# Optimization experiments

Measured on AMD Instinct MI355X. Metric: run time of the kernel, lower is better.

The kernel has to match this reference:

```python
import jax, jax.numpy as jnp
import numpy as np
from jax import lax

B = 8; IMG = 224; P = 16; D = 192; DEPTH = 8
H = IMG // P; W = H; L = H * W
D_IN = 384; D_STATE = 16; D_CONV = 4; DT_R = 12; NCLS = 1000
EPS = 1e-5


def _ln(x, w, b):
    m = x.mean(-1, keepdims=True)
    v = ((x - m) ** 2).mean(-1, keepdims=True)
    return (x - m) * lax.rsqrt(v + EPS) * w + b


def _mixer(seq, p):
    # seq: (B, L, D) -> Mamba selective-scan mixer
    xz = jnp.einsum('bld,ed->ble', seq, p['in_proj_w'])  # (B,L,2*D_IN)
    u, z = jnp.split(xz, 2, axis=-1)
    # causal depthwise conv1d over L
    uc = lax.conv_general_dilated(u.transpose(0, 2, 1), p['conv_w'][:, None, :], (1,),
                                  [(D_CONV - 1, 0)], feature_group_count=D_IN,
                                  dimension_numbers=('NCH', 'OIH', 'NCH'))
    u = jax.nn.silu(uc.transpose(0, 2, 1) + p['conv_b'])
    xdbl = jnp.einsum('bld,ed->ble', u, p['x_proj_w'])  # (B,L,DT_R+2*D_STATE)
    dt = xdbl[..., :DT_R]
    Bm = xdbl[..., DT_R:DT_R + D_STATE]
    Cm = xdbl[..., DT_R + D_STATE:]
    delta = jax.nn.softplus(jnp.einsum('blr,dr->bld', dt, p['dt_w']) + p['dt_b'])
    A = -jnp.exp(p['A_log'])  # (D_IN, D_STATE)

    def step(h, inp):
        d_t, B_t, C_t, u_t = inp  # (b,D_IN),(b,N),(b,N),(b,D_IN)
        h = h * jnp.exp(d_t[..., None] * A) + (d_t * u_t)[..., None] * B_t[:, None, :]
        return h, jnp.einsum('bdn,bn->bd', h, C_t)

    h0 = jnp.zeros((seq.shape[0], D_IN, D_STATE), seq.dtype)
    _, ys = lax.scan(step, h0, (delta.transpose(1, 0, 2), Bm.transpose(1, 0, 2),
                                Cm.transpose(1, 0, 2), u.transpose(1, 0, 2)))
    y = ys.transpose(1, 0, 2) + u * p['D']
    y = y * jax.nn.silu(z)
    return jnp.einsum('bld,cd->blc', y, p['out_proj_w'])


def _stack(seq, params):
    # Block: residual = residual + hidden; hidden = mixer(LN(residual))
    def body(carry, p):
        hidden, residual = carry
        residual = residual + hidden
        hidden = _mixer(_ln(residual, p['ln_w'], p['ln_b']), p)
        return (hidden, residual), None

    (hidden, residual), _ = lax.scan(body, (seq, jnp.zeros_like(seq)), params)
    return hidden + residual


def _forward(x, patch_w, patch_b, pe_ln_w, pe_ln_b, ln_w, ln_b, in_proj_w, conv_w,
             conv_b, x_proj_w, dt_w, dt_b, A_log, Dp, out_proj_w, out_norm_w,
             out_norm_b, head_ln_w, head_ln_b, head_w, head_b):
    b = x.shape[0]
    # patch embed: conv(stride=patch) + LayerNorm over channels
    feat = lax.conv_general_dilated(x, patch_w, (P, P), 'VALID',
                                    dimension_numbers=('NCHW', 'OIHW', 'NCHW'))
    feat = feat + patch_b[None, :, None, None]  # (B, D, H, W)
    feat = _ln(feat.transpose(0, 2, 3, 1), pe_ln_w, pe_ln_b).transpose(0, 3, 1, 2)
    # CrossScan: 4 directional unrollings
    x0 = feat.reshape(b, D, L)
    x1 = feat.transpose(0, 1, 3, 2).reshape(b, D, L)
    xs = jnp.stack([x0, x1, x0[..., ::-1], x1[..., ::-1]], axis=1)  # (B,4,D,L)
    dirs = xs.transpose(1, 0, 3, 2)  # (4,B,L,D)
    params = {'ln_w': ln_w, 'ln_b': ln_b, 'in_proj_w': in_proj_w, 'conv_w': conv_w,
              'conv_b': conv_b, 'x_proj_w': x_proj_w, 'dt_w': dt_w, 'dt_b': dt_b,
              'A_log': A_log, 'D': Dp, 'out_proj_w': out_proj_w}
    outs = jax.vmap(_stack)(dirs, params)  # (4,B,L,D)
    # CrossMerge
    ys = outs.transpose(1, 0, 3, 2)  # (B,4,D,L)
    ym = ys[:, 0:2] + ys[:, 2:4][..., ::-1]
    y = ym[:, 0] + ym[:, 1].reshape(b, D, W, H).transpose(0, 1, 3, 2).reshape(b, D, L)
    y = _ln(y.transpose(0, 2, 1), out_norm_w, out_norm_b)  # (B,L,D)
    y = _ln(y.reshape(b, H, W, D), head_ln_w, head_ln_b)
    return y.mean(axis=(1, 2)) @ head_w.T + head_b  # (B, NCLS)


def setup_inputs() -> dict:
    key = jax.random.key(0)
    ks = jax.random.split(key, 10)
    rn = lambda k, s, sc=0.02: jax.random.normal(k, s, jnp.float32) * sc
    A_init = jnp.broadcast_to(jnp.arange(1, D_STATE + 1, dtype=jnp.float32),
                              (4, DEPTH, D_IN, D_STATE))
    return {
        'x': jax.random.normal(ks[0], (B, 3, IMG, IMG), jnp.float32),
        'patch_w': rn(ks[1], (D, 3, P, P)),
        'patch_b': jnp.zeros((D,), jnp.float32),
        'pe_ln_w': jnp.ones((D,), jnp.float32),
        'pe_ln_b': jnp.zeros((D,), jnp.float32),
        'ln_w': jnp.ones((4, DEPTH, D), jnp.float32),
        'ln_b': jnp.zeros((4, DEPTH, D), jnp.float32),
        'in_proj_w': rn(ks[2], (4, DEPTH, 2 * D_IN, D)),
        'conv_w': rn(ks[3], (4, DEPTH, D_IN, D_CONV), 0.1),
        'conv_b': jnp.zeros((4, DEPTH, D_IN), jnp.float32),
        'x_proj_w': rn(ks[4], (4, DEPTH, DT_R + 2 * D_STATE, D_IN)),
        'dt_w': rn(ks[5], (4, DEPTH, D_IN, DT_R), 0.1),
        'dt_b': jnp.log(jnp.expm1(0.01)) + rn(ks[6], (4, DEPTH, D_IN), 0.02),
        'A_log': jnp.log(A_init),
        'Dp': jnp.ones((4, DEPTH, D_IN), jnp.float32),
        'out_proj_w': rn(ks[7], (4, DEPTH, D, D_IN)),
        'out_norm_w': jnp.ones((D,), jnp.float32),
        'out_norm_b': jnp.zeros((D,), jnp.float32),
        'head_ln_w': jnp.ones((D,), jnp.float32),
        'head_ln_b': jnp.zeros((D,), jnp.float32),
        'head_w': rn(ks[8], (NCLS, D)),
        'head_b': jnp.zeros((NCLS,), jnp.float32),
    }


def reference(x, patch_w, patch_b, pe_ln_w, pe_ln_b, ln_w, ln_b, in_proj_w, conv_w,
              conv_b, x_proj_w, dt_w, dt_b, A_log, Dp, out_proj_w, out_norm_w,
              out_norm_b, head_ln_w, head_ln_b, head_w, head_b):
    return _forward(x, patch_w, patch_b, pe_ln_w, pe_ln_b, ln_w, ln_b, in_proj_w,
                    conv_w, conv_b, x_proj_w, dt_w, dt_b, A_log, Dp, out_proj_w,
                    out_norm_w, out_norm_b, head_ln_w, head_ln_b, head_w, head_b)
```

## Files before the change

kernel.cpp:

```cpp
#include <hip/hip_runtime.h>

#define B_ 8
#define IMGSZ 224
#define PATCH 16
#define D_ 192
#define DEPTH_ 8
#define H_ 14
#define W_ 14
#define L_ 196
#define DIN 384
#define DSTATE 16
#define DCONV 4
#define DTR 12
#define NCLS_ 1000
#define EPS_ 1e-5f
#define ROWS_PER_DIR (B_*L_)
#define M_TOTAL (4*ROWS_PER_DIR)

typedef unsigned short ushort_t;
typedef unsigned int uint_t;
typedef __attribute__((ext_vector_type(8)))  short bf16x8;
typedef __attribute__((ext_vector_type(16))) float f32x16;

__device__ __forceinline__ ushort_t f2bf(float f) {
  uint_t u = __builtin_bit_cast(uint_t, f);
  u += 0x7fffu + ((u >> 16) & 1u);
  return (ushort_t)(u >> 16);
}
__device__ __forceinline__ float bf2f(ushort_t s) {
  uint_t u = ((uint_t)s) << 16;
  return __builtin_bit_cast(float, u);
}

__global__ __launch_bounds__(256) void k_cvt3(
    const float* __restrict__ s0, const float* __restrict__ s1,
    const float* __restrict__ s2, ushort_t* __restrict__ dst)
{
  int i = blockIdx.x*256 + threadIdx.x;
  if (i >= 1806336) return;
  const float* src;
  int off;
  if (i < 36864)        { src = s0; off = i; }
  else if (i < 1216512) { src = s1; off = i - 36864; }
  else                  { src = s2; off = i - 1216512; }
  float4 v = reinterpret_cast<const float4*>(src)[off];
  ushort4 o;
  o.x = f2bf(v.x); o.y = f2bf(v.y); o.z = f2bf(v.z); o.w = f2bf(v.w);
  reinterpret_cast<ushort4*>(dst)[i] = o;
}

__global__ __launch_bounds__(256) void k_cvt_xw(const float* __restrict__ src,
                                                ushort_t* __restrict__ dst)
{
  int idx = blockIdx.x*256 + threadIdx.x;
  if (idx >= 32*64*384) return;
  int g = idx / (64*384);
  int r = (idx / 384) % 64;
  int k = idx % 384;
  float v = (r < 44) ? src[((size_t)g*44 + r)*384 + k] : 0.f;
  dst[idx] = f2bf(v);
}

__global__ __launch_bounds__(256) void k_im2col(const float* __restrict__ x,
                                                ushort_t* __restrict__ Xp)
{
  int idx = blockIdx.x*256 + threadIdx.x;
  if (idx >= ROWS_PER_DIR*768) return;
  int row = idx / 768, k = idx - row*768;
  int b = row / L_, l = row - b*L_;
  int hh = l / W_, ww = l - hh*W_;
  int c = k >> 8, rem = k & 255, pi = rem >> 4, pj = rem & 15;
  float v = x[(((size_t)b*3 + c)*IMGSZ + hh*PATCH + pi)*IMGSZ + ww*PATCH + pj];
  Xp[idx] = f2bf(v);
}

template<int KT, int OBF>
__global__ __launch_bounds__(64) void k_gemm2(
    const ushort_t* __restrict__ X, const ushort_t* __restrict__ W,
    void* __restrict__ C, int N, int nb, int wstride, int rows_per_dir)
{
  int row0 = blockIdx.x*32, col0 = blockIdx.y*64;
  int dir = row0 / rows_per_dir;
  const ushort_t* Wp = W + (size_t)dir*wstride;
  int l = threadIdx.x;
  int r31 = l & 31, khalf = (l >> 5)*8;
  const ushort_t* aptr  = X  + (size_t)(row0 + r31)*KT + khalf;
  const ushort_t* b0ptr = Wp + (size_t)(col0 + r31)*KT + khalf;
  const ushort_t* b1ptr = b0ptr + (size_t)32*KT;
  f32x16 acc00 = {}, acc01 = {}, acc10 = {}, acc11 = {};
  #pragma unroll
  for (int k = 0; k < KT; k += 32) {
    bf16x8 a0 = *reinterpret_cast<const bf16x8*>(aptr + k);
    bf16x8 a1 = *reinterpret_cast<const bf16x8*>(aptr + k + 16);
    bf16x8 b00 = *reinterpret_cast<const bf16x8*>(b0ptr + k);
    bf16x8 b01 = *reinterpret_cast<const bf16x8*>(b0ptr + k + 16);
    bf16x8 b10 = *reinterpret_cast<const bf16x8*>(b1ptr + k);
    bf16x8 b11 = *reinterpret_cast<const bf16x8*>(b1ptr + k + 16);
    acc00 = __builtin_amdgcn_mfma_f32_32x32x16_bf16(a0, b00, acc00, 0, 0, 0);
    acc01 = __builtin_amdgcn_mfma_f32_32x32x16_bf16(a1, b01, acc01, 0, 0, 0);
    acc10 = __builtin_amdgcn_mfma_f32_32x32x16_bf16(a0, b10, acc10, 0, 0, 0);
    acc11 = __builtin_amdgcn_mfma_f32_32x32x16_bf16(a1, b11, acc11, 0, 0, 0);
  }
  int c0 = col0 + r31, c1 = col0 + 32 + r31;
  #pragma unroll
  for (int r = 0; r < 16; ++r) {
    int row = (r & 3) + 8*(r >> 2) + 4*(l >> 5);
    size_t base = (size_t)(row0 + row)*N;
    float v0 = acc00[r] + acc01[r];
    float v1 = acc10[r] + acc11[r];
    if (OBF) {
      ushort_t* crow = (ushort_t*)C + base;
      if (c0 < nb) crow[c0] = f2bf(v0);
      if (c1 < nb) crow[c1] = f2bf(v1);
    } else {
      float* crow = (float*)C + base;
      if (c0 < nb) crow[c0] = v0;
      if (c1 < nb) crow[c1] = v1;
    }
  }
}

__global__ __launch_bounds__(64) void k_peln(
    const float* __restrict__ Cp, const float* __restrict__ pb,
    const float* __restrict__ plw, const float* __restrict__ plb,
    const float* __restrict__ lnw, const float* __restrict__ lnb,
    float* __restrict__ residual, ushort_t* __restrict__ xln)
{
  int blk = blockIdx.x;
  int b = blk / L_, l = blk - b*L_;
  int hh = l / W_, ww = l - hh*W_;
  int lane = threadIdx.x;
  float v[3]; float s = 0.f;
  #pragma unroll
  for (int i = 0; i < 3; ++i) {
    int d = lane + i*64;
    float t = Cp[(size_t)blk*D_ + d] + pb[d];
    v[i] = t; s += t;
  }
  #pragma unroll
  for (int off = 32; off; off >>= 1) s += __shfl_xor(s, off);
  float m = s*(1.f/D_); float q = 0.f;
  #pragma unroll
  for (int i = 0; i < 3; ++i) { float dd = v[i]-m; q += dd*dd; }
  #pragma unroll
  for (int off = 32; off; off >>= 1) q += __shfl_xor(q, off);
  float inv = rsqrtf(q*(1.f/D_)+EPS_);
  float nv[3]; s = 0.f;
  #pragma unroll
  for (int i = 0; i < 3; ++i) {
    int d = lane + i*64;
    nv[i] = (v[i]-m)*inv*plw[d] + plb[d];
    s += nv[i];
  }
  #pragma unroll
  for (int off = 32; off; off >>= 1) s += __shfl_xor(s, off);
  float m2 = s*(1.f/D_); q = 0.f;
  #pragma unroll
  for (int i = 0; i < 3; ++i) { float dd = nv[i]-m2; q += dd*dd; }
  #pragma unroll
  for (int off = 32; off; off >>= 1) q += __shfl_xor(q, off);
  float inv2 = rsqrtf(q*(1.f/D_)+EPS_);
  int l1 = ww*W_ + hh;
  size_t rr[4];
  rr[0] = ((size_t)(0*B_+b))*L_ + l;
  rr[1] = ((size_t)(1*B_+b))*L_ + l1;
  rr[2] = ((size_t)(2*B_+b))*L_ + (L_-1-l);
  rr[3] = ((size_t)(3*B_+b))*L_ + (L_-1-l1);
  #pragma unroll
  for (int i = 0; i < 3; ++i) {
    int d = lane + i*64;
    float nrm = (nv[i]-m2)*inv2;
    #pragma unroll
    for (int k = 0; k < 4; ++k) {
      residual[rr[k]*D_+d] = nv[i];
      xln[rr[k]*D_+d] = f2bf(nrm*lnw[(size_t)(k*DEPTH_)*D_+d] + lnb[(size_t)(k*DEPTH_)*D_+d]);
    }
  }
}

__device__ __forceinline__ bf16x8 conv8(
    const ushort_t* __restrict__ xzb, int row, int l, int ch0,
    const float* __restrict__ scw, const float* __restrict__ scb)
{
  float acc[8];
  #pragma unroll
  for (int j = 0; j < 8; ++j) acc[j] = scb[ch0+j];
  #pragma unroll
  for (int t = 0; t < 4; ++t) {
    int lt = l - 3 + t;
    if (lt >= 0) {
      bf16x8 xv = *reinterpret_cast<const bf16x8*>(xzb + (size_t)(row-3+t)*768 + ch0);
      #pragma unroll
      for (int j = 0; j < 8; ++j)
        acc[j] += bf2f((ushort_t)xv[j]) * scw[(ch0+j)*4 + t];
    }
  }
  bf16x8 o;
  #pragma unroll
  for (int j = 0; j < 8; ++j) {
    float uv = acc[j] / (1.f + __expf(-acc[j]));
    o[j] = (short)f2bf(uv);
  }
  return o;
}

__global__ __launch_bounds__(64) void k_xprojc(
    const ushort_t* __restrict__ xzb,
    const float* __restrict__ cw, const float* __restrict__ cb,
    const ushort_t* __restrict__ xw, float* __restrict__ xdbl, int layer)
{
  int row0 = blockIdx.x*32;
  int dir = row0 / ROWS_PER_DIR;
  __shared__ __align__(16) float scw[DIN*DCONV];
  __shared__ float scb[DIN];
  int tid = threadIdx.x;
  {
    const float* cwp = cw + (size_t)(dir*DEPTH_+layer)*DIN*DCONV;
    const float* cbp = cb + (size_t)(dir*DEPTH_+layer)*DIN;
    for (int i = tid; i < 384; i += 64) {
      reinterpret_cast<float4*>(scw)[i] = reinterpret_cast<const float4*>(cwp)[i];
      scb[i] = cbp[i];
    }
  }
  __syncthreads();
  int r31 = tid & 31, khalf = (tid >> 5)*8;
  int row = row0 + r31;
  int l = row % L_;
  const ushort_t* b0ptr = xw + (size_t)(dir*DEPTH_+layer)*64*384 + (size_t)r31*384 + khalf;
  const ushort_t* b1ptr = b0ptr + (size_t)32*384;
  f32x16 acc00 = {}, acc01 = {}, acc10 = {}, acc11 = {};
  #pragma unroll 4
  for (int k = 0; k < DIN; k += 32) {
    bf16x8 a0 = conv8(xzb, row, l, k + khalf, scw, scb);
    bf16x8 a1 = conv8(xzb, row, l, k + khalf + 16, scw, scb);
    bf16x8 b00 = *reinterpret_cast<const bf16x8*>(b0ptr + k);
    bf16x8 b01 = *reinterpret_cast<const bf16x8*>(b0ptr + k + 16);
    bf16x8 b10 = *reinterpret_cast<const bf16x8*>(b1ptr + k);
    bf16x8 b11 = *reinterpret_cast<const bf16x8*>(b1ptr + k + 16);
    acc00 = __builtin_amdgcn_mfma_f32_32x32x16_bf16(a0, b00, acc00, 0, 0, 0);
    acc01 = __builtin_amdgcn_mfma_f32_32x32x16_bf16(a1, b01, acc01, 0, 0, 0);
    acc10 = __builtin_amdgcn_mfma_f32_32x32x16_bf16(a0, b10, acc10, 0, 0, 0);
    acc11 = __builtin_amdgcn_mfma_f32_32x32x16_bf16(a1, b11, acc11, 0, 0, 0);
  }
  int c0 = r31, c1 = 32 + r31;
  #pragma unroll
  for (int r = 0; r < 16; ++r) {
    int rr = (r & 3) + 8*(r >> 2) + 4*(tid >> 5);
    float* crow = xdbl + (size_t)(row0 + rr)*44;
    crow[c0] = acc00[r] + acc01[r];
    if (c1 < 44) crow[c1] = acc10[r] + acc11[r];
  }
}

#define SCHUNK 14
#define NCHUNK 14
__global__ __launch_bounds__(256, 3) void k_scan(
    const ushort_t* __restrict__ xzb, const float* __restrict__ xdbl,
    const float* __restrict__ Alog, const float* __restrict__ Dp,
    const float* __restrict__ dtw, const float* __restrict__ dtb,
    const float* __restrict__ cw, const float* __restrict__ cb,
    ushort_t* __restrict__ yg, int layer)
{
  int blk = blockIdx.x;
  int kdir = blk / (B_*24);
  int rem = blk % (B_*24);
  int b = rem / 24, dc = rem % 24;
  int tid = threadIdx.x;
  int st = tid & 15, ch = tid >> 4;
  size_t pl = (size_t)(kdir*DEPTH_+layer)*DIN + dc*16 + ch;
  float a = -expf(Alog[pl*DSTATE + st]);
  size_t rowbase = ((size_t)kdir*B_ + b)*L_;

  int ll = tid >> 4, cc = tid & 15;
  bool ldr = tid < 224;
  size_t plc = (size_t)(kdir*DEPTH_+layer)*DIN + dc*16 + cc;
  float Dv3 = Dp[plc];
  float dwt[12]; float dbias = dtb[plc];
  #pragma unroll
  for (int i = 0; i < 3; ++i)
    ((float4*)dwt)[i] = ((const float4*)(dtw + plc*DTR))[i];
  float cwv[4]; float cbv = cb[plc];
  *((float4*)cwv) = *((const float4*)(cw + plc*DCONV));

  __shared__ __align__(16) float sd[16][20], su[16][20], sB[16][20],
                                 sC[16][20], sz[16][20];
  __shared__ __align__(16) float sp[SCHUNK][16][20];

  float rd=0.f, ru=0.f, rB=0.f, rC=0.f, rz=0.f;
  if (ldr) {
    int l0 = ll;
    int row = (int)(rowbase + l0);
    float xv[12];
    #pragma unroll
    for (int i = 0; i < 3; ++i) ((float4*)xv)[i] = ((const float4*)(xdbl + (size_t)row*44))[i];
    float acc = dbias;
    #pragma unroll
    for (int t = 0; t < DTR; ++t) acc += xv[t]*dwt[t];
    rd = (acc > 20.f) ? acc : log1pf(__expf(acc));
    float ua = cbv;
    #pragma unroll
    for (int t = 0; t < 4; ++t) {
      int lt = l0 - 3 + t;
      if (lt >= 0) ua += bf2f(xzb[(size_t)(row-3+t)*768 + dc*16 + cc]) * cwv[t];
    }
    ru = ua / (1.f + __expf(-ua));
    rB = xdbl[(size_t)row*44 + DTR + cc];
    rC = xdbl[(size_t)row*44 + DTR + DSTATE + cc];
    rz = bf2f(xzb[(size_t)row*768 + DIN + dc*16 + cc]);
  }

  float h = 0.f;
  for (int chk = 0; chk < NCHUNK; ++chk) {
    if (ldr) { sd[cc][ll]=rd; su[cc][ll]=ru; sB[cc][ll]=rB; sC[cc][ll]=rC; sz[cc][ll]=rz; }
    __syncthreads();
    if (chk+1 < NCHUNK && ldr) {
      int l0 = (chk+1)*SCHUNK + ll;
      int row = (int)(rowbase + l0);
      float xv[12];
      #pragma unroll
      for (int i = 0; i < 3; ++i) ((float4*)xv)[i] = ((const float4*)(xdbl + (size_t)row*44))[i];
      float acc = dbias;
      #pragma unroll
      for (int t = 0; t < DTR; ++t) acc += xv[t]*dwt[t];
      rd = (acc > 20.f) ? acc : log1pf(__expf(acc));
      float ua = cbv;
      #pragma unroll
      for (int t = 0; t < 4; ++t) {
        int lt = l0 - 3 + t;
        if (lt >= 0) ua += bf2f(xzb[(size_t)(row-3+t)*768 + dc*16 + cc]) * cwv[t];
      }
      ru = ua / (1.f + __expf(-ua));
      rB = xdbl[(size_t)row*44 + DTR + cc];
      rC = xdbl[(size_t)row*44 + DTR + DSTATE + cc];
      rz = bf2f(xzb[(size_t)row*768 + DIN + dc*16 + cc]);
    }
    float dlv[16], ulv[16], Bvv[16], Cvv[16];
    #pragma unroll
    for (int i = 0; i < 4; ++i) {
      ((float4*)dlv)[i] = ((const float4*)&sd[ch][0])[i];
      ((float4*)ulv)[i] = ((const float4*)&su[ch][0])[i];
      ((float4*)Bvv)[i] = ((const float4*)&sB[st][0])[i];
      ((float4*)Cvv)[i] = ((const float4*)&sC[st][0])[i];
    }
    float E[SCHUNK];
    #pragma unroll
    for (int l = 0; l < SCHUNK; ++l) E[l] = __expf(dlv[l]*a);
    #pragma unroll
    for (int l = 0; l < SCHUNK; ++l) {
      h = h*E[l] + dlv[l]*ulv[l]*Bvv[l];
      sp[l][ch][st] = h*Cvv[l];
    }
    __syncthreads();
    if (ldr) {
      float pv[16];
      #pragma unroll
      for (int i = 0; i < 4; ++i)
        ((float4*)pv)[i] = ((const float4*)&sp[ll][cc][0])[i];
      float s = 0.f;
      #pragma unroll
      for (int i = 0; i < 16; ++i) s += pv[i];
      float ul = su[cc][ll];
      float z  = sz[cc][ll];
      float yv = (s + ul*Dv3) * (z / (1.f + __expf(-z)));
      yg[(rowbase + chk*SCHUNK + ll)*DIN + dc*16 + cc] = f2bf(yv);
    }
    __syncthreads();
  }
}

template<int LAST>
__global__ __launch_bounds__(384) void k_outln(
    const ushort_t* __restrict__ X, const ushort_t* __restrict__ W,
    float* __restrict__ residual,
    const float* __restrict__ lnw, const float* __restrict__ lnb,
    ushort_t* __restrict__ xln, int layer)
{
  int row0 = blockIdx.x*32;
  int dir = row0 / ROWS_PER_DIR;
  const ushort_t* Wp = W + (size_t)dir*(DEPTH_*D_*DIN);
  int tid = threadIdx.x;
  int wv = tid >> 6;
  int l  = tid & 63;
  int col0 = wv*32;
  int r31 = l & 31, khalf = (l >> 5)*8;
  const ushort_t* aptr = X  + (size_t)(row0 + r31)*DIN + khalf;
  const ushort_t* bptr = Wp + (size_t)(col0 + r31)*DIN + khalf;
  f32x16 acc0 = {}, acc1 = {};
  #pragma unroll
  for (int k = 0; k < DIN; k += 32) {
    bf16x8 a0 = *reinterpret_cast<const bf16x8*>(aptr + k);
    bf16x8 b0 = *reinterpret_cast<const bf16x8*>(bptr + k);
    bf16x8 a1 = *reinterpret_cast<const bf16x8*>(aptr + k + 16);
    bf16x8 b1 = *reinterpret_cast<const bf16x8*>(bptr + k + 16);
    acc0 = __builtin_amdgcn_mfma_f32_32x32x16_bf16(a0, b0, acc0, 0, 0, 0);
    acc1 = __builtin_amdgcn_mfma_f32_32x32x16_bf16(a1, b1, acc1, 0, 0, 0);
  }
  __shared__ __align__(16) float Cs[32][196];
  __shared__ float sred[32][12], qred[32][12], sm[32], si[32];
  #pragma unroll
  for (int r = 0; r < 16; ++r) {
    int row = (r & 3) + 8*(r >> 2) + 4*(l >> 5);
    Cs[row][col0 + r31] = acc0[r] + acc1[r];
  }
  __syncthreads();
  int rr = tid / 12, jj = tid - rr*12;
  int c0 = jj*16;
  float* resrow = residual + (size_t)(row0+rr)*D_ + c0;
  float v[16];
  float s = 0.f, q = 0.f;
  #pragma unroll
  for (int i = 0; i < 16; i += 4) {
    float4 rv = *reinterpret_cast<const float4*>(resrow + i);
    float4 cv = *reinterpret_cast<const float4*>(&Cs[rr][c0 + i]);
    v[i+0] = rv.x + cv.x; v[i+1] = rv.y + cv.y;
    v[i+2] = rv.z + cv.z; v[i+3] = rv.w + cv.w;
  }
  #pragma unroll
  for (int i = 0; i < 16; ++i) { s += v[i]; q += v[i]*v[i]; }
  #pragma unroll
  for (int i = 0; i < 16; i += 4) {
    float4 o = make_float4(v[i], v[i+1], v[i+2], v[i+3]);
    *reinterpret_cast<float4*>(resrow + i) = o;
  }
  if (!LAST) {
    sred[rr][jj] = s; qred[rr][jj] = q;
    __syncthreads();
    if (tid < 32) {
      float S = 0.f, Q = 0.f;
      #pragma unroll
      for (int j = 0; j < 12; ++j) { S += sred[tid][j]; Q += qred[tid][j]; }
      float m = S*(1.f/D_);
      float var = Q*(1.f/D_) - m*m;
      sm[tid] = m; si[tid] = rsqrtf(var + EPS_);
    }
    __syncthreads();
    float m = sm[rr], inv = si[rr];
    const float* w = lnw + (size_t)(dir*DEPTH_ + layer + 1)*D_ + c0;
    const float* bb = lnb + (size_t)(dir*DEPTH_ + layer + 1)*D_ + c0;
    ushort_t* xrow = xln + (size_t)(row0+rr)*D_ + c0;
    #pragma unroll
    for (int i = 0; i < 16; ++i)
      xrow[i] = f2bf((v[i]-m)*inv*w[i] + bb[i]);
  }
}

__global__ __launch_bounds__(64) void k_combine(
    const float* __restrict__ res,
    const float* __restrict__ onw, const float* __restrict__ onb,
    const float* __restrict__ hlw, const float* __restrict__ hlb,
    float* __restrict__ ynorm)
{
  int blk = blockIdx.x;
  int b = blk / L_, l = blk % L_;
  int hh = l / W_, ww = l % W_;
  int l1 = ww*W_ + hh;
  size_t r0 = ((size_t)(0*B_+b))*L_ + l;
  size_t r1 = ((size_t)(1*B_+b))*L_ + l1;
  size_t r2 = ((size_t)(2*B_+b))*L_ + (L_-1-l);
  size_t r3 = ((size_t)(3*B_+b))*L_ + (L_-1-l1);
  int lane = threadIdx.x;
  float v[3]; float s = 0.f;
  #pragma unroll
  for (int i=0;i<3;i++){
    int d = lane + i*64;
    float t = res[r0*D_+d] + res[r1*D_+d] + res[r2*D_+d] + res[r3*D_+d];
    v[i]=t; s+=t;
  }
  #pragma unroll
  for (int off=32;off;off>>=1) s += __shfl_xor(s,off);
  float m = s*(1.f/D_); float q=0.f;
  #pragma unroll
  for (int i=0;i<3;i++){ float dd=v[i]-m; q+=dd*dd; }
  #pragma unroll
  for (int off=32;off;off>>=1) q += __shfl_xor(q,off);
  float inv = rsqrtf(q*(1.f/D_)+EPS_);
  float v2[3]; s = 0.f;
  #pragma unroll
  for (int i=0;i<3;i++){ int d=lane+i*64; float t=(v[i]-m)*inv*onw[d]+onb[d]; v2[i]=t; s+=t; }
  #pragma unroll
  for (int off=32;off;off>>=1) s += __shfl_xor(s,off);
  float m2 = s*(1.f/D_); q=0.f;
  #pragma unroll
  for (int i=0;i<3;i++){ float dd=v2[i]-m2; q+=dd*dd; }
  #pragma unroll
  for (int off=32;off;off>>=1) q += __shfl_xor(q,off);
  float inv2 = rsqrtf(q*(1.f/D_)+EPS_);
  #pragma unroll
  for (int i=0;i<3;i++){ int d=lane+i*64; ynorm[((size_t)b*L_+l)*D_+d] = (v2[i]-m2)*inv2*hlw[d]+hlb[d]; }
}

__global__ __launch_bounds__(192) void k_mean(const float* __restrict__ ynorm, float* __restrict__ ybar)
{
  int b = blockIdx.x, d = threadIdx.x;
  float s = 0.f;
  for (int l = 0; l < L_; ++l) s += ynorm[((size_t)b*L_+l)*D_ + d];
  ybar[b*D_+d] = s * (1.f/L_);
}

__global__ __launch_bounds__(256) void k_head(
    const float* __restrict__ ybar, const float* __restrict__ hw, const float* __restrict__ hb,
    float* __restrict__ out)
{
  __shared__ float ys[D_];
  int b = blockIdx.x >> 2;
  int c = (blockIdx.x & 3)*256 + threadIdx.x;
  for (int i = threadIdx.x; i < D_; i += 256) ys[i] = ybar[b*D_+i];
  __syncthreads();
  if (c < NCLS_) {
    float acc = hb[c];
    const float* wr = hw + (size_t)c*D_;
    for (int dd = 0; dd < D_; dd += 4) {
      float4 a4 = *reinterpret_cast<const float4*>(&ys[dd]);
      float4 b4 = *reinterpret_cast<const float4*>(&wr[dd]);
      acc += a4.x*b4.x + a4.y*b4.y + a4.z*b4.z + a4.w*b4.w;
    }
    out[(size_t)b*NCLS_ + c] = acc;
  }
}

extern "C" void kernel_launch(void* const* d_in, const int* in_sizes, int n_in,
                              void* d_out, int out_size, void* d_ws, size_t ws_size,
                              hipStream_t stream)
{
  const float* x          = (const float*)d_in[0];
  const float* patch_w    = (const float*)d_in[1];
  const float* patch_b    = (const float*)d_in[2];
  const float* pe_ln_w    = (const float*)d_in[3];
  const float* pe_ln_b    = (const float*)d_in[4];
  const float* ln_w       = (const float*)d_in[5];
  const float* ln_b       = (const float*)d_in[6];
  const float* in_proj_w  = (const float*)d_in[7];
  const float* conv_w     = (const float*)d_in[8];
  const float* conv_b     = (const float*)d_in[9];
  const float* x_proj_w   = (const float*)d_in[10];
  const float* dt_w       = (const float*)d_in[11];
  const float* dt_b       = (const float*)d_in[12];
  const float* A_log      = (const float*)d_in[13];
  const float* Dp         = (const float*)d_in[14];
  const float* out_proj_w = (const float*)d_in[15];
  const float* out_norm_w = (const float*)d_in[16];
  const float* out_norm_b = (const float*)d_in[17];
  const float* head_ln_w  = (const float*)d_in[18];
  const float* head_ln_b  = (const float*)d_in[19];
  const float* head_w     = (const float*)d_in[20];
  const float* head_b     = (const float*)d_in[21];
  float* out = (float*)d_out;

  float* ws = (float*)d_ws;
  float*    residual = ws;
  ushort_t* xz_bf    = (ushort_t*)(residual + 1204224);
  float*    xdbl     = (float*)(xz_bf + 4816896);
  ushort_t* yg_bf    = (ushort_t*)(xdbl + 275968);
  ushort_t* xln_bf   = yg_bf + 2408448;
  ushort_t* wbf      = xln_bf + 1204224;
  ushort_t* pw_bf    = wbf;
  ushort_t* inw_bf   = wbf + 147456;
  ushort_t* outw_bf  = inw_bf + 4718592;
  ushort_t* xw_bf    = outw_bf + 2359296;
  ushort_t* Xp       = xz_bf;
  float*    C_patch  = (float*)(xz_bf + 1204224);
  float*    ynorm    = (float*)yg_bf;
  float*    ybar     = ynorm + 301056;

  k_cvt3<<<(1806336+255)/256, 256, 0, stream>>>(patch_w, in_proj_w, out_proj_w, wbf);
  k_cvt_xw<<<(32*64*384+255)/256, 256, 0, stream>>>(x_proj_w, xw_bf);

  k_im2col<<<(ROWS_PER_DIR*768+255)/256, 256, 0, stream>>>(x, Xp);
  k_gemm2<768,0><<<dim3(ROWS_PER_DIR/32, 3), 64, 0, stream>>>(
      Xp, pw_bf, C_patch, D_, D_, 0, ROWS_PER_DIR);
  k_peln<<<ROWS_PER_DIR, 64, 0, stream>>>(C_patch, patch_b, pe_ln_w, pe_ln_b,
                                          ln_w, ln_b, residual, xln_bf);

  for (int layer = 0; layer < DEPTH_; ++layer) {
    k_gemm2<192,1><<<dim3(M_TOTAL/32, 12), 64, 0, stream>>>(
        xln_bf, inw_bf + (size_t)layer*768*D_, xz_bf, 768, 768, DEPTH_*768*D_, ROWS_PER_DIR);
    k_xprojc<<<M_TOTAL/32, 64, 0, stream>>>(
        xz_bf, conv_w, conv_b, xw_bf, xdbl, layer);
    k_scan<<<4*B_*24, 256, 0, stream>>>(
        xz_bf, xdbl, A_log, Dp, dt_w, dt_b, conv_w, conv_b, yg_bf, layer);
    if (layer < DEPTH_-1)
      k_outln<0><<<M_TOTAL/32, 384, 0, stream>>>(
          yg_bf, outw_bf, residual, ln_w, ln_b, xln_bf, layer);
    else
      k_outln<1><<<M_TOTAL/32, 384, 0, stream>>>(
          yg_bf, outw_bf, residual, ln_w, ln_b, xln_bf, layer);
  }

  k_combine<<<B_*L_, 64, 0, stream>>>(residual, out_norm_w, out_norm_b,
                                      head_ln_w, head_ln_b, ynorm);
  k_mean<<<B_, 192, 0, stream>>>(ynorm, ybar);
  k_head<<<B_*4, 256, 0, stream>>>(ybar, head_w, head_b, out);
}
```

Before: 783.2 us.

## Split depthwise conv into its own kernel and reuse materialized u in x_proj and scan

The causal conv plus SiLU, previously recomputed inside the x_proj MFMA kernel and again in the scan, now runs once in a dedicated elementwise kernel that writes u to a new bf16 workspace buffer. x_proj then runs through the generic k_gemm2 template, and the scan reads u directly instead of recomputing the conv. This removes redundant conv work and the LDS setup in the fused GEMM. In exchange it adds a kernel launch and an extra write and read of the u tensor per layer, and it depends on k_gemm2 handling N=44 correctly.

Result: faster. 703.1 us (-10.2%).

```diff
diff --git a/kernel.cpp b/kernel.cpp
--- a/kernel.cpp
+++ b/kernel.cpp
@@ -178,21 +178,32 @@
   }
 }
 
-__device__ __forceinline__ bf16x8 conv8(
-    const ushort_t* __restrict__ xzb, int row, int l, int ch0,
-    const float* __restrict__ scw, const float* __restrict__ scb)
-{
+__global__ __launch_bounds__(256) void k_conv(
+    const ushort_t* __restrict__ xzb, const float* __restrict__ cw,
+    const float* __restrict__ cb, ushort_t* __restrict__ ub, int layer)
+{
+  int idx = blockIdx.x*256 + threadIdx.x;
+  if (idx >= M_TOTAL*48) return;
+  int row = idx / 48, c8 = (idx - row*48)*8;
+  int kdir = row / ROWS_PER_DIR;
+  int l = row % L_;
+  size_t pbase = (size_t)(kdir*DEPTH_+layer)*DIN + c8;
+  float wv[32];
+  #pragma unroll
+  for (int i = 0; i < 8; ++i)
+    ((float4*)wv)[i] = ((const float4*)(cw + pbase*DCONV))[i];
   float acc[8];
   #pragma unroll
-  for (int j = 0; j < 8; ++j) acc[j] = scb[ch0+j];
-  #pragma unroll
-  for (int t = 0; t < 4; ++t) {
+  for (int i = 0; i < 2; ++i)
+    ((float4*)acc)[i] = ((const float4*)(cb + pbase))[i];
+  #pragma unroll
+  for (int t = 0; t < DCONV; ++t) {
     int lt = l - 3 + t;
     if (lt >= 0) {
-      bf16x8 xv = *reinterpret_cast<const bf16x8*>(xzb + (size_t)(row-3+t)*768 + ch0);
+      bf16x8 xv = *reinterpret_cast<const bf16x8*>(xzb + (size_t)(row-3+t)*768 + c8);
       #pragma unroll
       for (int j = 0; j < 8; ++j)
-        acc[j] += bf2f((ushort_t)xv[j]) * scw[(ch0+j)*4 + t];
+        acc[j] += bf2f((ushort_t)xv[j]) * wv[j*4 + t];
     }
   }
   bf16x8 o;
@@ -201,64 +212,16 @@
     float uv = acc[j] / (1.f + __expf(-acc[j]));
     o[j] = (short)f2bf(uv);
   }
-  return o;
-}
-
-__global__ __launch_bounds__(64) void k_xprojc(
-    const ushort_t* __restrict__ xzb,
-    const float* __restrict__ cw, const float* __restrict__ cb,
-    const ushort_t* __restrict__ xw, float* __restrict__ xdbl, int layer)
-{
-  int row0 = blockIdx.x*32;
-  int dir = row0 / ROWS_PER_DIR;
-  __shared__ __align__(16) float scw[DIN*DCONV];
-  __shared__ float scb[DIN];
-  int tid = threadIdx.x;
-  {
-    const float* cwp = cw + (size_t)(dir*DEPTH_+layer)*DIN*DCONV;
-    const float* cbp = cb + (size_t)(dir*DEPTH_+layer)*DIN;
-    for (int i = tid; i < 384; i += 64) {
-      reinterpret_cast<float4*>(scw)[i] = reinterpret_cast<const float4*>(cwp)[i];
-      scb[i] = cbp[i];
-    }
-  }
-  __syncthreads();
-  int r31 = tid & 31, khalf = (tid >> 5)*8;
-  int row = row0 + r31;
-  int l = row % L_;
-  const ushort_t* b0ptr = xw + (size_t)(dir*DEPTH_+layer)*64*384 + (size_t)r31*384 + khalf;
-  const ushort_t* b1ptr = b0ptr + (size_t)32*384;
-  f32x16 acc00 = {}, acc01 = {}, acc10 = {}, acc11 = {};
-  #pragma unroll 4
-  for (int k = 0; k < DIN; k += 32) {
-    bf16x8 a0 = conv8(xzb, row, l, k + khalf, scw, scb);
-    bf16x8 a1 = conv8(xzb, row, l, k + khalf + 16, scw, scb);
-    bf16x8 b00 = *reinterpret_cast<const bf16x8*>(b0ptr + k);
-    bf16x8 b01 = *reinterpret_cast<const bf16x8*>(b0ptr + k + 16);
-    bf16x8 b10 = *reinterpret_cast<const bf16x8*>(b1ptr + k);
-    bf16x8 b11 = *reinterpret_cast<const bf16x8*>(b1ptr + k + 16);
-    acc00 = __builtin_amdgcn_mfma_f32_32x32x16_bf16(a0, b00, acc00, 0, 0, 0);
-    acc01 = __builtin_amdgcn_mfma_f32_32x32x16_bf16(a1, b01, acc01, 0, 0, 0);
-    acc10 = __builtin_amdgcn_mfma_f32_32x32x16_bf16(a0, b10, acc10, 0, 0, 0);
-    acc11 = __builtin_amdgcn_mfma_f32_32x32x16_bf16(a1, b11, acc11, 0, 0, 0);
-  }
-  int c0 = r31, c1 = 32 + r31;
-  #pragma unroll
-  for (int r = 0; r < 16; ++r) {
-    int rr = (r & 3) + 8*(r >> 2) + 4*(tid >> 5);
-    float* crow = xdbl + (size_t)(row0 + rr)*44;
-    crow[c0] = acc00[r] + acc01[r];
-    if (c1 < 44) crow[c1] = acc10[r] + acc11[r];
-  }
+  *reinterpret_cast<bf16x8*>(ub + (size_t)row*DIN + c8) = o;
 }
 
 #define SCHUNK 14
 #define NCHUNK 14
 __global__ __launch_bounds__(256, 3) void k_scan(
-    const ushort_t* __restrict__ xzb, const float* __restrict__ xdbl,
+    const ushort_t* __restrict__ ub, const float* __restrict__ xdbl,
+    const ushort_t* __restrict__ xzb,
     const float* __restrict__ Alog, const float* __restrict__ Dp,
     const float* __restrict__ dtw, const float* __restrict__ dtb,
-    const float* __restrict__ cw, const float* __restrict__ cb,
     ushort_t* __restrict__ yg, int layer)
 {
   int blk = blockIdx.x;
@@ -279,8 +242,6 @@
   #pragma unroll
   for (int i = 0; i < 3; ++i)
     ((float4*)dwt)[i] = ((const float4*)(dtw + plc*DTR))[i];
-  float cwv[4]; float cbv = cb[plc];
-  *((float4*)cwv) = *((const float4*)(cw + plc*DCONV));
 
   __shared__ __align__(16) float sd[16][20], su[16][20], sB[16][20],
                                  sC[16][20], sz[16][20];
@@ -288,25 +249,18 @@
 
   float rd=0.f, ru=0.f, rB=0.f, rC=0.f, rz=0.f;
   if (ldr) {
-    int l0 = ll;
-    int row = (int)(rowbase + l0);
+    size_t r = rowbase + ll;
     float xv[12];
     #pragma unroll
-    for (int i = 0; i < 3; ++i) ((float4*)xv)[i] = ((const float4*)(xdbl + (size_t)row*44))[i];
+    for (int i = 0; i < 3; ++i) ((float4*)xv)[i] = ((const float4*)(xdbl + r*44))[i];
     float acc = dbias;
     #pragma unroll
     for (int t = 0; t < DTR; ++t) acc += xv[t]*dwt[t];
     rd = (acc > 20.f) ? acc : log1pf(__expf(acc));
-    float ua = cbv;
-    #pragma unroll
-    for (int t = 0; t < 4; ++t) {
-      int lt = l0 - 3 + t;
-      if (lt >= 0) ua += bf2f(xzb[(size_t)(row-3+t)*768 + dc*16 + cc]) * cwv[t];
-    }
-    ru = ua / (1.f + __expf(-ua));
-    rB = xdbl[(size_t)row*44 + DTR + cc];
-    rC = xdbl[(size_t)row*44 + DTR + DSTATE + cc];
-    rz = bf2f(xzb[(size_t)row*768 + DIN + dc*16 + cc]);
+    ru = bf2f(ub[r*DIN + dc*16 + cc]);
+    rB = xdbl[r*44 + DTR + cc];
+    rC = xdbl[r*44 + DTR + DSTATE + cc];
+    rz = bf2f(xzb[r*768 + DIN + dc*16 + cc]);
   }
 
   float h = 0.f;
@@ -314,25 +268,18 @@
     if (ldr) { sd[cc][ll]=rd; su[cc][ll]=ru; sB[cc][ll]=rB; sC[cc][ll]=rC; sz[cc][ll]=rz; }
     __syncthreads();
     if (chk+1 < NCHUNK && ldr) {
-      int l0 = (chk+1)*SCHUNK + ll;
-      int row = (int)(rowbase + l0);
+      size_t r = rowbase + (chk+1)*SCHUNK + ll;
       float xv[12];
       #pragma unroll
-      for (int i = 0; i < 3; ++i) ((float4*)xv)[i] = ((const float4*)(xdbl + (size_t)row*44))[i];
+      for (int i = 0; i < 3; ++i) ((float4*)xv)[i] = ((const float4*)(xdbl + r*44))[i];
       float acc = dbias;
       #pragma unroll
       for (int t = 0; t < DTR; ++t) acc += xv[t]*dwt[t];
       rd = (acc > 20.f) ? acc : log1pf(__expf(acc));
-      float ua = cbv;
-      #pragma unroll
-      for (int t = 0; t < 4; ++t) {
-        int lt = l0 - 3 + t;
-        if (lt >= 0) ua += bf2f(xzb[(size_t)(row-3+t)*768 + dc*16 + cc]) * cwv[t];
-      }
-      ru = ua / (1.f + __expf(-ua));
-      rB = xdbl[(size_t)row*44 + DTR + cc];
-      rC = xdbl[(size_t)row*44 + DTR + DSTATE + cc];
-      rz = bf2f(xzb[(size_t)row*768 + DIN + dc*16 + cc]);
+      ru = bf2f(ub[r*DIN + dc*16 + cc]);
+      rB = xdbl[r*44 + DTR + cc];
+      rC = xdbl[r*44 + DTR + DSTATE + cc];
+      rz = bf2f(xzb[r*768 + DIN + dc*16 + cc]);
     }
     float dlv[16], ulv[16], Bvv[16], Cvv[16];
     #pragma unroll
@@ -549,7 +496,8 @@
   float* ws = (float*)d_ws;
   float*    residual = ws;
   ushort_t* xz_bf    = (ushort_t*)(residual + 1204224);
-  float*    xdbl     = (float*)(xz_bf + 4816896);
+  ushort_t* u_bf     = xz_bf + 4816896;
+  float*    xdbl     = (float*)(u_bf + 2408448);
   ushort_t* yg_bf    = (ushort_t*)(xdbl + 275968);
   ushort_t* xln_bf   = yg_bf + 2408448;
   ushort_t* wbf      = xln_bf + 1204224;
@@ -574,10 +522,11 @@
   for (int layer = 0; layer < DEPTH_; ++layer) {
     k_gemm2<192,1><<<dim3(M_TOTAL/32, 12), 64, 0, stream>>>(
         xln_bf, inw_bf + (size_t)layer*768*D_, xz_bf, 768, 768, DEPTH_*768*D_, ROWS_PER_DIR);
-    k_xprojc<<<M_TOTAL/32, 64, 0, stream>>>(
-        xz_bf, conv_w, conv_b, xw_bf, xdbl, layer);
+    k_conv<<<(M_TOTAL*48+255)/256, 256, 0, stream>>>(xz_bf, conv_w, conv_b, u_bf, layer);
+    k_gemm2<384,0><<<dim3(M_TOTAL/32, 1), 64, 0, stream>>>(
+        u_bf, xw_bf + (size_t)layer*64*384, xdbl, 44, 44, DEPTH_*64*384, ROWS_PER_DIR);
     k_scan<<<4*B_*24, 256, 0, stream>>>(
-        xz_bf, xdbl, A_log, Dp, dt_w, dt_b, conv_w, conv_b, yg_bf, layer);
+        u_bf, xdbl, xz_bf, A_log, Dp, dt_w, dt_b, yg_bf, layer);
     if (layer < DEPTH_-1)
       k_outln<0><<<M_TOTAL/32, 384, 0, stream>>>(
           yg_bf, outw_bf, residual, ln_w, ln_b, xln_bf, layer);
```
